# Performance work log

Hardware: AMD Instinct MI355X
Metric: run time of the kernel (lower is better)

Reference implementation:

```python
import jax, jax.numpy as jnp
import numpy as np

B, S, D = 4, 2048, 1024   # batch, seq_len, size
K = 4                     # max_choice
A = 2                     # activate_choice (== default forward choices)


def setup_inputs() -> dict:
    key = jax.random.key(0)
    ks = jax.random.split(key, 8)
    sc = 0.02  # weight init scale
    return {
        "x": jax.random.normal(ks[0], (B, S, D), jnp.float32),
        "Wm": jax.random.normal(ks[1], (A, D, D), jnp.float32) * sc,   # Memory expert weights
        "bm": jnp.zeros((A, D), jnp.float32),
        "ln_g": jnp.ones((D,), jnp.float32),                            # shared LayerNorm (self.lim)
        "ln_b": jnp.zeros((D,), jnp.float32),
        "Wg": jax.random.normal(ks[2], (D, K), jnp.float32) * sc,       # Linker gate
        "bg": jnp.zeros((K,), jnp.float32),
        "We": jax.random.normal(ks[3], (K, D, D), jnp.float32) * sc,    # Linker experts
        "be": jnp.zeros((K, D), jnp.float32),
        "Wfit": jax.random.normal(ks[4], ((A + 1) * D, D), jnp.float32) * sc,
        "bfit": jnp.zeros((D,), jnp.float32),
        "choices": A,
    }


def _layer_norm(x, g, b, eps=1e-5):
    m = jnp.mean(x, axis=-1, keepdims=True)
    v = jnp.mean((x - m) ** 2, axis=-1, keepdims=True)
    return (x - m) * jax.lax.rsqrt(v + eps) * g + b


def reference(x, Wm, bm, ln_g, ln_b, Wg, bg, We, be, Wfit, bfit, choices):
    # Triple-nested per-token loop vectorized: the in-place += means each
    # choice's Memory expert sees the x already updated by previous choices,
    # i.e. sequentially over `choices`: x <- x + LN(Memory_c(x)).
    for c in range(choices):
        mem = jnp.einsum('bsd,de->bse', x, Wm[c]) + bm[c]
        x = x + _layer_norm(mem, ln_g, ln_b)

    # Linker: gate over max_choice experts, pick top-`choices`, concat outputs.
    logits = jnp.einsum('bsd,dk->bsk', x, Wg) + bg          # [B,S,K]
    _, idx = jax.lax.top_k(logits, choices)                  # [B,S,A]
    eo = jnp.einsum('bsd,kde->bske', x, We) + be             # [B,S,K,D]
    sel = jnp.take_along_axis(eo, idx[..., None], axis=2)    # [B,S,A,D]
    link = sel.reshape(sel.shape[0], sel.shape[1], -1)       # [B,S,A*D]

    h = jnp.concatenate([link, x], axis=-1)                  # [B,S,(A+1)*D]
    h = jnp.einsum('bsf,fd->bsd', h, Wfit) + bfit
    h = _layer_norm(h, ln_g, ln_b)
    return jax.nn.gelu(h, approximate=False)
```

## Files before the change

kernel.cpp:

```cpp
#include <hip/hip_runtime.h>
#include <hip/hip_bf16.h>
#include <math.h>

typedef __bf16 bf16x8 __attribute__((ext_vector_type(8)));
typedef float  f32x4  __attribute__((ext_vector_type(4)));
typedef unsigned int   u32;
typedef unsigned short u16;
typedef u16 u16x8 __attribute__((ext_vector_type(8)));

#define D_ 1024
#define M_ 8192

static __device__ __forceinline__ u16 f2bf(float f) {
  u32 x = __float_as_uint(f);
  return (u16)((x + 0x7fffu + ((x >> 16) & 1u)) >> 16);
}
static __device__ __forceinline__ float bf2f(u16 s) {
  union { u32 b; float f; } u; u.b = ((u32)s) << 16; return u.f;
}
static __device__ __forceinline__ void gload16(const u16* g, u16* l) {
  __builtin_amdgcn_global_load_lds((const __attribute__((address_space(1))) u32*)g,
                                   (__attribute__((address_space(3))) u32*)l, 16, 0, 0);
}


__global__ __launch_bounds__(256) void pack_A_mem(const float* __restrict__ x, u16* __restrict__ dst) {
  int gid = blockIdx.x * 256 + threadIdx.x;
  int G = gid & 2047;
  int kblk = (gid >> 11) & 31;
  int mblk = gid >> 16;
  int rrow = G >> 3, gp = G & 7;
  int kg = gp ^ (rrow & 7);
  int region = kblk >> 4;
  int k = ((kblk & 15) * 8 + kg) * 8;
  const float* src = x + ((size_t)mblk * 256 + rrow) * D_ + k;
  f32x4 v0 = *reinterpret_cast<const f32x4*>(src);
  f32x4 v1 = *reinterpret_cast<const f32x4*>(src + 4);
  u16x8 o8;
#pragma unroll
  for (int j = 0; j < 4; ++j) {
    u16 h0 = f2bf(v0[j]); o8[j]     = region ? f2bf(v0[j] - bf2f(h0)) : h0;
    u16 h1 = f2bf(v1[j]); o8[4 + j] = region ? f2bf(v1[j] - bf2f(h1)) : h1;
  }
  *reinterpret_cast<u16x8*>(dst + (size_t)gid * 8) = o8;
}

__global__ __launch_bounds__(256) void pack_W_mem(const float* __restrict__ W, u16* __restrict__ dst) {
  __shared__ float tile[64][129];
  int bidx = blockIdx.x;
  int nt = bidx & 7, kt = (bidx >> 3) & 15, c = bidx >> 7;
  const float* Ws = W + ((size_t)c * D_ + kt * 64) * D_ + nt * 128;
#pragma unroll
  for (int rep = 0; rep < 32; ++rep) {
    int idx = rep * 256 + threadIdx.x;
    tile[idx >> 7][idx & 127] = Ws[(size_t)(idx >> 7) * D_ + (idx & 127)];
  }
  __syncthreads();
#pragma unroll
  for (int rep = 0; rep < 8; ++rep) {
    int gi = rep * 256 + threadIdx.x;
    int region = gi >> 10;
    int G = gi & 1023;
    int col = G >> 3, gp = G & 7;
    int kg = gp ^ (col & 7);
    u16x8 o8;
#pragma unroll
    for (int j = 0; j < 8; ++j) {
      float v = tile[kg * 8 + j][col];
      u16 h = f2bf(v);
      o8[j] = region ? f2bf(v - bf2f(h)) : h;
    }
    int kblk = region * 16 + kt;
    size_t off = ((((size_t)c * 8 + nt) * 32 + kblk) * 1024 + col * 8 + gp) * 8;
    *reinterpret_cast<u16x8*>(dst + off) = o8;
  }
}

__global__ __launch_bounds__(256) void pack_W_plain(const float* __restrict__ W, u16* __restrict__ dst, int KBLK) {
  __shared__ float tile[64][129];
  int bidx = blockIdx.x;
  int nt = bidx & 7;
  int t2 = bidx >> 3;
  int kt = t2 % KBLK;
  int e  = t2 / KBLK;
  const float* Ws = W + ((size_t)e * KBLK * 64 + kt * 64) * D_ + nt * 128;
#pragma unroll
  for (int rep = 0; rep < 32; ++rep) {
    int idx = rep * 256 + threadIdx.x;
    tile[idx >> 7][idx & 127] = Ws[(size_t)(idx >> 7) * D_ + (idx & 127)];
  }
  __syncthreads();
#pragma unroll
  for (int rep = 0; rep < 4; ++rep) {
    int gi = rep * 256 + threadIdx.x;
    int col = gi >> 3, gp = gi & 7;
    int kg = gp ^ (col & 7);
    u16x8 o8;
#pragma unroll
    for (int j = 0; j < 8; ++j) o8[j] = f2bf(tile[kg * 8 + j][col]);
    size_t off = ((((size_t)e * 8 + nt) * KBLK + kt) * 1024 + col * 8 + gp) * 8;
    *reinterpret_cast<u16x8*>(dst + off) = o8;
  }
}


__global__ __launch_bounds__(256) void ln1_pack(const float* __restrict__ xin, const float* __restrict__ mem,
                                                const float* __restrict__ bm, const float* __restrict__ g,
                                                const float* __restrict__ b, float* __restrict__ xout,
                                                u16* __restrict__ apack) {
  int row = blockIdx.x, tid = threadIdx.x;
  __shared__ float yrow[1024];
  __shared__ float red[8];
  f32x4 mv = *reinterpret_cast<const f32x4*>(mem + (size_t)row * D_ + tid * 4);
  f32x4 bi = *reinterpret_cast<const f32x4*>(bm + tid * 4);
  float a[4]; float s = 0.f, ss = 0.f;
#pragma unroll
  for (int i = 0; i < 4; ++i) { a[i] = mv[i] + bi[i]; s += a[i]; ss += a[i] * a[i]; }
#pragma unroll
  for (int o = 1; o < 64; o <<= 1) { s += __shfl_xor(s, o); ss += __shfl_xor(ss, o); }
  int wv = tid >> 6, ln = tid & 63;
  if (ln == 0) { red[wv] = s; red[4 + wv] = ss; }
  __syncthreads();
  float S = red[0] + red[1] + red[2] + red[3];
  float SS = red[4] + red[5] + red[6] + red[7];
  float mean = S * (1.f / 1024.f);
  float var = SS * (1.f / 1024.f) - mean * mean;
  float rs = rsqrtf(var + 1e-5f);
  f32x4 g4 = *reinterpret_cast<const f32x4*>(g + tid * 4);
  f32x4 b4 = *reinterpret_cast<const f32x4*>(b + tid * 4);
  f32x4 xv = *reinterpret_cast<const f32x4*>(xin + (size_t)row * D_ + tid * 4);
  f32x4 o4;
#pragma unroll
  for (int i = 0; i < 4; ++i) o4[i] = xv[i] + (a[i] - mean) * rs * g4[i] + b4[i];
  *reinterpret_cast<f32x4*>(xout + (size_t)row * D_ + tid * 4) = o4;
  *reinterpret_cast<f32x4*>(yrow + tid * 4) = o4;
  __syncthreads();
  int region = tid >> 7;
  int q = tid & 127;
  int kblk = region * 16 + (q >> 3);
  int kg = q & 7;
  int rrow = row & 255, mblk = row >> 8;
  const float* ys = yrow + q * 8;
  u16x8 o8;
#pragma unroll
  for (int j = 0; j < 8; ++j) {
    float v = ys[j]; u16 h = f2bf(v);
    o8[j] = region ? f2bf(v - bf2f(h)) : h;
  }
  size_t off = (((size_t)mblk * 32 + kblk) * 2048 + rrow * 8 + (kg ^ (rrow & 7))) * 8;
  *reinterpret_cast<u16x8*>(apack + off) = o8;
}

__global__ __launch_bounds__(256) void ln2_gate_pack(const float* __restrict__ xin, const float* __restrict__ mem,
                                                     const float* __restrict__ bm1, const float* __restrict__ g,
                                                     const float* __restrict__ b, const float* __restrict__ Wg,
                                                     const float* __restrict__ bg, u16* __restrict__ apack,
                                                     u16* __restrict__ hpack, int2* __restrict__ idx) {
  int row = blockIdx.x, tid = threadIdx.x;
  __shared__ float yrow[1024];
  __shared__ float red[8];
  __shared__ float gred[16];
  f32x4 mv = *reinterpret_cast<const f32x4*>(mem + (size_t)row * D_ + tid * 4);
  f32x4 bi = *reinterpret_cast<const f32x4*>(bm1 + tid * 4);
  float a[4]; float s = 0.f, ss = 0.f;
#pragma unroll
  for (int i = 0; i < 4; ++i) { a[i] = mv[i] + bi[i]; s += a[i]; ss += a[i] * a[i]; }
#pragma unroll
  for (int o = 1; o < 64; o <<= 1) { s += __shfl_xor(s, o); ss += __shfl_xor(ss, o); }
  int wv = tid >> 6, ln = tid & 63;
  if (ln == 0) { red[wv] = s; red[4 + wv] = ss; }
  __syncthreads();
  float S = red[0] + red[1] + red[2] + red[3];
  float SS = red[4] + red[5] + red[6] + red[7];
  float mean = S * (1.f / 1024.f);
  float var = SS * (1.f / 1024.f) - mean * mean;
  float rs = rsqrtf(var + 1e-5f);
  f32x4 g4 = *reinterpret_cast<const f32x4*>(g + tid * 4);
  f32x4 b4 = *reinterpret_cast<const f32x4*>(b + tid * 4);
  f32x4 xv = *reinterpret_cast<const f32x4*>(xin + (size_t)row * D_ + tid * 4);
  f32x4 o4;
#pragma unroll
  for (int i = 0; i < 4; ++i) o4[i] = xv[i] + (a[i] - mean) * rs * g4[i] + b4[i];
  *reinterpret_cast<f32x4*>(yrow + tid * 4) = o4;
  float p0 = 0.f, p1 = 0.f, p2 = 0.f, p3 = 0.f;
#pragma unroll
  for (int i = 0; i < 4; ++i) {
    f32x4 w = *reinterpret_cast<const f32x4*>(Wg + (size_t)(tid * 4 + i) * 4);
    p0 += o4[i] * w[0]; p1 += o4[i] * w[1]; p2 += o4[i] * w[2]; p3 += o4[i] * w[3];
  }
#pragma unroll
  for (int o = 1; o < 64; o <<= 1) {
    p0 += __shfl_xor(p0, o); p1 += __shfl_xor(p1, o);
    p2 += __shfl_xor(p2, o); p3 += __shfl_xor(p3, o);
  }
  if (ln == 0) { gred[wv * 4] = p0; gred[wv * 4 + 1] = p1; gred[wv * 4 + 2] = p2; gred[wv * 4 + 3] = p3; }
  __syncthreads();
  if (tid == 0) {
    float lg[4];
#pragma unroll
    for (int c = 0; c < 4; ++c) lg[c] = gred[c] + gred[4 + c] + gred[8 + c] + gred[12 + c] + bg[c];
    int i0 = 0; float v0 = lg[0];
#pragma unroll
    for (int k = 1; k < 4; ++k) if (lg[k] > v0) { v0 = lg[k]; i0 = k; }
    int i1 = -1; float v1 = -3.4e38f;
#pragma unroll
    for (int k = 0; k < 4; ++k) if (k != i0 && lg[k] > v1) { v1 = lg[k]; i1 = k; }
    idx[row] = make_int2(i0, i1);
  }
  int q = tid & 127;
  int kblk = q >> 3, kg = q & 7;
  int rrow = row & 255, mblk = row >> 8;
  const float* ys = yrow + q * 8;
  u16x8 o8;
#pragma unroll
  for (int j = 0; j < 8; ++j) o8[j] = f2bf(ys[j]);
  int pos = rrow * 8 + (kg ^ (rrow & 7));
  if (tid < 128) {
    *reinterpret_cast<u16x8*>(apack + (((size_t)mblk * 16 + kblk) * 2048 + pos) * 8) = o8;
  } else {
    *reinterpret_cast<u16x8*>(hpack + (((size_t)mblk * 48 + 32 + kblk) * 2048 + pos) * 8) = o8;
  }
}

__global__ __launch_bounds__(256) void final_ln_gelu(const float* __restrict__ fit, const float* __restrict__ bfit,
                                                     const float* __restrict__ g, const float* __restrict__ b,
                                                     float* __restrict__ out) {
  int row = blockIdx.x, tid = threadIdx.x;
  f32x4 hv = *reinterpret_cast<const f32x4*>(fit + (size_t)row * D_ + tid * 4);
  f32x4 bi = *reinterpret_cast<const f32x4*>(bfit + tid * 4);
  float a[4]; float s = 0.f, ss = 0.f;
#pragma unroll
  for (int i = 0; i < 4; ++i) { a[i] = hv[i] + bi[i]; s += a[i]; ss += a[i] * a[i]; }
#pragma unroll
  for (int o = 1; o < 64; o <<= 1) { s += __shfl_xor(s, o); ss += __shfl_xor(ss, o); }
  __shared__ float red[8];
  int wv = tid >> 6, ln = tid & 63;
  if (ln == 0) { red[wv] = s; red[4 + wv] = ss; }
  __syncthreads();
  float S = red[0] + red[1] + red[2] + red[3];
  float SS = red[4] + red[5] + red[6] + red[7];
  float mean = S * (1.f / 1024.f);
  float var = SS * (1.f / 1024.f) - mean * mean;
  float rs = rsqrtf(var + 1e-5f);
  f32x4 g4 = *reinterpret_cast<const f32x4*>(g + tid * 4);
  f32x4 b4 = *reinterpret_cast<const f32x4*>(b + tid * 4);
  f32x4 o4;
#pragma unroll
  for (int i = 0; i < 4; ++i) {
    float y = (a[i] - mean) * rs * g4[i] + b4[i];
    o4[i] = 0.5f * y * (1.f + erff(y * 0.70710678118654752f));
  }
  *reinterpret_cast<f32x4*>(out + (size_t)row * D_ + tid * 4) = o4;
}

#define MFMA(a, b, c) __builtin_amdgcn_mfma_f32_16x16x32_bf16(a, b, c, 0, 0, 0)

template<int MEMFOLD, int EPI>
__global__ __launch_bounds__(512, 1) void gemm8(const u16* __restrict__ A, const u16* __restrict__ B,
                                                float* __restrict__ C, u16* __restrict__ hp,
                                                const int2* __restrict__ idx, const float* __restrict__ be,
                                                int KIT, int AKB, int BKB) {
  __shared__ __align__(16) u16 lds[3][24576];
  const int tid = threadIdx.x;
  const int wid = tid >> 6, l = tid & 63;
  const int wm = wid >> 1, wn = wid & 1;
  const int lk = l >> 4, l15 = l & 15;
  const int bid = blockIdx.x;
  const int mblk = bid & 31;
  const int nblk = (bid >> 5) & 7;
  const int e    = bid >> 8;

  const u16* Ablob = A + (size_t)mblk * AKB * 16384;
  const u16* Bblob = B + ((size_t)e * 8 + nblk) * BKB * 8192;

  f32x4 acc[4][4];
#pragma unroll
  for (int i = 0; i < 4; ++i)
#pragma unroll
    for (int j = 0; j < 4; ++j) acc[i][j] = (f32x4){0.f, 0.f, 0.f, 0.f};

  auto amap = [&](int it) -> int {
    if (!MEMFOLD) return it;
    int kb = (int)((unsigned)it / 3u), sub = it - kb * 3;
    return kb + (sub == 2 ? 16 : 0);
  };
  auto bmap = [&](int it) -> int {
    if (!MEMFOLD) return it;
    int kb = (int)((unsigned)it / 3u), sub = it - kb * 3;
    return kb + (sub == 1 ? 16 : 0);
  };

  auto stageA0 = [&](int s, int it) {
    const u16* As = Ablob + (size_t)amap(it) * 16384;
#pragma unroll
    for (int r = 0; r < 3; ++r) {
      int u = r * 512 + tid;
      gload16(As + (size_t)u * 8, &lds[s][u * 8]);
    }
  };
  auto stageA1B = [&](int s, int it) {
    const u16* As = Ablob + (size_t)amap(it) * 16384;
    const u16* Bs = Bblob + (size_t)bmap(it) * 8192;
    int u = 3 * 512 + tid;
    gload16(As + (size_t)u * 8, &lds[s][u * 8]);
#pragma unroll
    for (int r = 0; r < 2; ++r) {
      int v = r * 512 + tid;
      gload16(Bs + (size_t)v * 8, &lds[s][16384 + v * 8]);
    }
  };
  auto ldA = [&](int s, int mi, int ks) -> bf16x8 {
    int r = wm * 64 + mi * 16 + l15;
    int gp = (ks * 4 + lk) ^ (r & 7);
    return *reinterpret_cast<const bf16x8*>(&lds[s][(r * 8 + gp) * 8]);
  };
  auto ldB = [&](int s, int ni, int ks) -> bf16x8 {
    int c = wn * 64 + ni * 16 + l15;
    int gp = (ks * 4 + lk) ^ (c & 7);
    return *reinterpret_cast<const bf16x8*>(&lds[s][16384 + (c * 8 + gp) * 8]);
  };

  stageA0(0, 0); stageA1B(0, 0);
  stageA0(1, 1); stageA1B(1, 1);
  asm volatile("s_waitcnt vmcnt(6)" ::: "memory");
  asm volatile("s_barrier" ::: "memory");

  int cur = 0;
  for (int t = 0; t < KIT; ++t) {
    int nxt = cur + 2; if (nxt >= 3) nxt -= 3;
    bool pf = (t + 2) < KIT;
    bf16x8 A0, A1, A2, A3, B0, B1, B2, B3;
    A0 = ldA(cur, 0, 0); A1 = ldA(cur, 1, 0); A2 = ldA(cur, 2, 0); A3 = ldA(cur, 3, 0);
    B0 = ldB(cur, 0, 0); B1 = ldB(cur, 1, 0); B2 = ldB(cur, 2, 0); B3 = ldB(cur, 3, 0);
    if (pf) stageA0(nxt, t + 2);
    __builtin_amdgcn_s_setprio(1);
    acc[0][0] = MFMA(A0, B0, acc[0][0]); acc[1][0] = MFMA(A1, B0, acc[1][0]);
    acc[2][0] = MFMA(A2, B0, acc[2][0]); acc[3][0] = MFMA(A3, B0, acc[3][0]);
    acc[0][1] = MFMA(A0, B1, acc[0][1]); acc[1][1] = MFMA(A1, B1, acc[1][1]);
    acc[2][1] = MFMA(A2, B1, acc[2][1]); acc[3][1] = MFMA(A3, B1, acc[3][1]);
    acc[0][2] = MFMA(A0, B2, acc[0][2]); acc[1][2] = MFMA(A1, B2, acc[1][2]);
    acc[2][2] = MFMA(A2, B2, acc[2][2]); acc[3][2] = MFMA(A3, B2, acc[3][2]);
    acc[0][3] = MFMA(A0, B3, acc[0][3]); acc[1][3] = MFMA(A1, B3, acc[1][3]);
    acc[2][3] = MFMA(A2, B3, acc[2][3]); acc[3][3] = MFMA(A3, B3, acc[3][3]);
    __builtin_amdgcn_s_setprio(0);
    asm volatile("s_barrier" ::: "memory");
    A0 = ldA(cur, 0, 1); A1 = ldA(cur, 1, 1); A2 = ldA(cur, 2, 1); A3 = ldA(cur, 3, 1);
    B0 = ldB(cur, 0, 1); B1 = ldB(cur, 1, 1); B2 = ldB(cur, 2, 1); B3 = ldB(cur, 3, 1);
    if (pf) stageA1B(nxt, t + 2);
    __builtin_amdgcn_s_setprio(1);
    acc[0][0] = MFMA(A0, B0, acc[0][0]); acc[1][0] = MFMA(A1, B0, acc[1][0]);
    acc[2][0] = MFMA(A2, B0, acc[2][0]); acc[3][0] = MFMA(A3, B0, acc[3][0]);
    acc[0][1] = MFMA(A0, B1, acc[0][1]); acc[1][1] = MFMA(A1, B1, acc[1][1]);
    acc[2][1] = MFMA(A2, B1, acc[2][1]); acc[3][1] = MFMA(A3, B1, acc[3][1]);
    acc[0][2] = MFMA(A0, B2, acc[0][2]); acc[1][2] = MFMA(A1, B2, acc[1][2]);
    acc[2][2] = MFMA(A2, B2, acc[2][2]); acc[3][2] = MFMA(A3, B2, acc[3][2]);
    acc[0][3] = MFMA(A0, B3, acc[0][3]); acc[1][3] = MFMA(A1, B3, acc[1][3]);
    acc[2][3] = MFMA(A2, B3, acc[2][3]); acc[3][3] = MFMA(A3, B3, acc[3][3]);
    __builtin_amdgcn_s_setprio(0);
    if (pf) { asm volatile("s_waitcnt vmcnt(6)" ::: "memory"); }
    else    { asm volatile("s_waitcnt vmcnt(0)" ::: "memory"); }
    asm volatile("s_barrier" ::: "memory");
    cur += 1; if (cur >= 3) cur -= 3;
  }

  if (EPI == 0) {
#pragma unroll
    for (int mi = 0; mi < 4; ++mi) {
#pragma unroll
      for (int jj = 0; jj < 4; ++jj) {
        int row = mblk * 256 + wm * 64 + mi * 16 + lk * 4 + jj;
        float* Crow = C + (size_t)row * D_ + nblk * 128 + wn * 64 + l15;
#pragma unroll
        for (int ni = 0; ni < 4; ++ni) Crow[ni * 16] = acc[mi][ni][jj];
      }
    }
  } else {
#pragma unroll
    for (int mi = 0; mi < 4; ++mi) {
      int rbase = mblk * 256 + wm * 64 + mi * 16 + lk * 4;
      int2 rid[4];
#pragma unroll
      for (int jj = 0; jj < 4; ++jj) rid[jj] = idx[rbase + jj];
#pragma unroll
      for (int ni = 0; ni < 4; ++ni) {
        int col = nblk * 128 + wn * 64 + ni * 16 + l15;
        float bev = be[(size_t)e * D_ + col];
#pragma unroll
        for (int jj = 0; jj < 4; ++jj) {
          int slot = (rid[jj].x == e) ? 0 : ((rid[jj].y == e) ? 1 : -1);
          if (slot >= 0) {
            int row = rbase + jj;
            int rrow = row & 255;
            int kh = slot * D_ + col;
            int kblk = kh >> 6;
            int kg = (kh >> 3) & 7;
            size_t off = (((size_t)mblk * 48 + kblk) * 2048 + rrow * 8 + (kg ^ (rrow & 7))) * 8 + (kh & 7);
            hp[off] = f2bf(acc[mi][ni][jj] + bev);
          }
        }
      }
    }
  }
}

extern "C" void kernel_launch(void* const* d_in, const int* in_sizes, int n_in,
                              void* d_out, int out_size, void* d_ws, size_t ws_size,
                              hipStream_t stream) {
  const float* x_in = (const float*)d_in[0];
  const float* Wm   = (const float*)d_in[1];
  const float* bm   = (const float*)d_in[2];
  const float* ln_g = (const float*)d_in[3];
  const float* ln_b = (const float*)d_in[4];
  const float* Wg   = (const float*)d_in[5];
  const float* bg   = (const float*)d_in[6];
  const float* We   = (const float*)d_in[7];
  const float* be   = (const float*)d_in[8];
  const float* Wfit = (const float*)d_in[9];
  const float* bfit = (const float*)d_in[10];
  float* out = (float*)d_out;

  char* ws = (char*)d_ws;
  size_t off = 0;
  auto alloc = [&](size_t bytes) -> void* {
    void* p = ws + off; off += (bytes + 255) & ~(size_t)255; return p;
  };
  float* x1      = (float*)alloc((size_t)M_ * D_ * 4);
  float* memb    = (float*)alloc((size_t)M_ * D_ * 4);
  u16* AmemPack  = (u16*)alloc((size_t)32 * 32 * 2048 * 16);
  u16* AplainPk  = (u16*)alloc((size_t)32 * 16 * 2048 * 16);
  u16* Hpack     = (u16*)alloc((size_t)32 * 48 * 2048 * 16);
  u16* WmPack    = (u16*)alloc((size_t)2 * 8 * 32 * 1024 * 16);
  u16* WePack    = (u16*)alloc((size_t)4 * 8 * 16 * 1024 * 16);
  u16* WfPack    = (u16*)alloc((size_t)8 * 48 * 1024 * 16);
  int2* idxb     = (int2*)alloc((size_t)M_ * 8);

  pack_W_mem  <<<256, 256, 0, stream>>>(Wm, WmPack);
  pack_W_plain<<<512, 256, 0, stream>>>(We, WePack, 16);
  pack_W_plain<<<384, 256, 0, stream>>>(Wfit, WfPack, 48);

  pack_A_mem<<<8192, 256, 0, stream>>>(x_in, AmemPack);
  gemm8<1, 0><<<256, 512, 0, stream>>>(AmemPack, WmPack, memb, nullptr, nullptr, nullptr, 48, 32, 32);
  ln1_pack<<<8192, 256, 0, stream>>>(x_in, memb, bm, ln_g, ln_b, x1, AmemPack);
  gemm8<1, 0><<<256, 512, 0, stream>>>(AmemPack, WmPack + (size_t)2097152, memb,
                                       nullptr, nullptr, nullptr, 48, 32, 32);
  ln2_gate_pack<<<8192, 256, 0, stream>>>(x1, memb, bm + D_, ln_g, ln_b, Wg, bg, AplainPk, Hpack, idxb);

  gemm8<0, 1><<<1024, 512, 0, stream>>>(AplainPk, WePack, nullptr, Hpack, idxb, be, 16, 16, 16);

  gemm8<0, 0><<<256, 512, 0, stream>>>(Hpack, WfPack, memb, nullptr, nullptr, nullptr, 48, 48, 48);

  final_ln_gelu<<<8192, 256, 0, stream>>>(memb, bfit, ln_g, ln_b, out);
}
```

Before: 424.6 us.

## Split GEMM tile staging into four chunks interleaved with MFMA phases

Replaces the two prefetch stages per K-iteration with four smaller chunks (two A halves and two B pieces). Each chunk is issued between finer-grained MFMA groups, and B fragment LDS reads are split so that only two B fragments are loaded before each half of the MFMAs. The goal is to spread global-to-LDS traffic and LDS reads more evenly across the compute, so the matrix units are fed more steadily. In exchange, each iteration now has several extra s_barrier and lgkmcnt(0) waits, which could add synchronisation stalls.

```diff
diff --git a/kernel.cpp b/kernel.cpp
--- a/kernel.cpp
+++ b/kernel.cpp
@@ -290,22 +290,16 @@
     return kb + (sub == 1 ? 16 : 0);
   };
 
-  auto stageA0 = [&](int s, int it) {
-    const u16* As = Ablob + (size_t)amap(it) * 16384;
-#pragma unroll
-    for (int r = 0; r < 3; ++r) {
-      int u = r * 512 + tid;
-      gload16(As + (size_t)u * 8, &lds[s][u * 8]);
-    }
-  };
-  auto stageA1B = [&](int s, int it) {
-    const u16* As = Ablob + (size_t)amap(it) * 16384;
-    const u16* Bs = Bblob + (size_t)bmap(it) * 8192;
-    int u = 3 * 512 + tid;
-    gload16(As + (size_t)u * 8, &lds[s][u * 8]);
-#pragma unroll
-    for (int r = 0; r < 2; ++r) {
-      int v = r * 512 + tid;
+  auto stageChunk = [&](int s, int it, int c) {
+    if (c <= 1) {
+      const u16* As = Ablob + (size_t)amap(it) * 16384;
+      int u0 = c * 1024 + tid;
+      int u1 = u0 + 512;
+      gload16(As + (size_t)u0 * 8, &lds[s][u0 * 8]);
+      gload16(As + (size_t)u1 * 8, &lds[s][u1 * 8]);
+    } else {
+      const u16* Bs = Bblob + (size_t)bmap(it) * 8192;
+      int v = (c - 2) * 512 + tid;
       gload16(Bs + (size_t)v * 8, &lds[s][16384 + v * 8]);
     }
   };
@@ -320,8 +314,8 @@
     return *reinterpret_cast<const bf16x8*>(&lds[s][16384 + (c * 8 + gp) * 8]);
   };
 
-  stageA0(0, 0); stageA1B(0, 0);
-  stageA0(1, 1); stageA1B(1, 1);
+  stageChunk(0, 0, 0); stageChunk(0, 0, 1); stageChunk(0, 0, 2); stageChunk(0, 0, 3);
+  stageChunk(1, 1, 0); stageChunk(1, 1, 1); stageChunk(1, 1, 2); stageChunk(1, 1, 3);
   asm volatile("s_waitcnt vmcnt(6)" ::: "memory");
   asm volatile("s_barrier" ::: "memory");
 
@@ -331,13 +325,22 @@
     bool pf = (t + 2) < KIT;
     bf16x8 A0, A1, A2, A3, B0, B1, B2, B3;
     A0 = ldA(cur, 0, 0); A1 = ldA(cur, 1, 0); A2 = ldA(cur, 2, 0); A3 = ldA(cur, 3, 0);
-    B0 = ldB(cur, 0, 0); B1 = ldB(cur, 1, 0); B2 = ldB(cur, 2, 0); B3 = ldB(cur, 3, 0);
-    if (pf) stageA0(nxt, t + 2);
+    B0 = ldB(cur, 0, 0); B1 = ldB(cur, 1, 0);
+    if (pf) stageChunk(nxt, t + 2, 0);
+    asm volatile("s_barrier" ::: "memory");
+    asm volatile("s_waitcnt lgkmcnt(0)" ::: "memory");
     __builtin_amdgcn_s_setprio(1);
     acc[0][0] = MFMA(A0, B0, acc[0][0]); acc[1][0] = MFMA(A1, B0, acc[1][0]);
     acc[2][0] = MFMA(A2, B0, acc[2][0]); acc[3][0] = MFMA(A3, B0, acc[3][0]);
     acc[0][1] = MFMA(A0, B1, acc[0][1]); acc[1][1] = MFMA(A1, B1, acc[1][1]);
     acc[2][1] = MFMA(A2, B1, acc[2][1]); acc[3][1] = MFMA(A3, B1, acc[3][1]);
+    __builtin_amdgcn_s_setprio(0);
+    asm volatile("s_barrier" ::: "memory");
+    B2 = ldB(cur, 2, 0); B3 = ldB(cur, 3, 0);
+    if (pf) stageChunk(nxt, t + 2, 1);
+    asm volatile("s_barrier" ::: "memory");
+    asm volatile("s_waitcnt lgkmcnt(0)" ::: "memory");
+    __builtin_amdgcn_s_setprio(1);
     acc[0][2] = MFMA(A0, B2, acc[0][2]); acc[1][2] = MFMA(A1, B2, acc[1][2]);
     acc[2][2] = MFMA(A2, B2, acc[2][2]); acc[3][2] = MFMA(A3, B2, acc[3][2]);
     acc[0][3] = MFMA(A0, B3, acc[0][3]); acc[1][3] = MFMA(A1, B3, acc[1][3]);
@@ -345,13 +348,22 @@
     __builtin_amdgcn_s_setprio(0);
     asm volatile("s_barrier" ::: "memory");
     A0 = ldA(cur, 0, 1); A1 = ldA(cur, 1, 1); A2 = ldA(cur, 2, 1); A3 = ldA(cur, 3, 1);
-    B0 = ldB(cur, 0, 1); B1 = ldB(cur, 1, 1); B2 = ldB(cur, 2, 1); B3 = ldB(cur, 3, 1);
-    if (pf) stageA1B(nxt, t + 2);
+    B0 = ldB(cur, 0, 1); B1 = ldB(cur, 1, 1);
+    if (pf) stageChunk(nxt, t + 2, 2);
+    asm volatile("s_barrier" ::: "memory");
+    asm volatile("s_waitcnt lgkmcnt(0)" ::: "memory");
     __builtin_amdgcn_s_setprio(1);
     acc[0][0] = MFMA(A0, B0, acc[0][0]); acc[1][0] = MFMA(A1, B0, acc[1][0]);
     acc[2][0] = MFMA(A2, B0, acc[2][0]); acc[3][0] = MFMA(A3, B0, acc[3][0]);
     acc[0][1] = MFMA(A0, B1, acc[0][1]); acc[1][1] = MFMA(A1, B1, acc[1][1]);
     acc[2][1] = MFMA(A2, B1, acc[2][1]); acc[3][1] = MFMA(A3, B1, acc[3][1]);
+    __builtin_amdgcn_s_setprio(0);
+    asm volatile("s_barrier" ::: "memory");
+    B2 = ldB(cur, 2, 1); B3 = ldB(cur, 3, 1);
+    if (pf) stageChunk(nxt, t + 2, 3);
+    asm volatile("s_barrier" ::: "memory");
+    asm volatile("s_waitcnt lgkmcnt(0)" ::: "memory");
+    __builtin_amdgcn_s_setprio(1);
     acc[0][2] = MFMA(A0, B2, acc[0][2]); acc[1][2] = MFMA(A1, B2, acc[1][2]);
     acc[2][2] = MFMA(A2, B2, acc[2][2]); acc[3][2] = MFMA(A3, B2, acc[3][2]);
     acc[0][3] = MFMA(A0, B3, acc[0][3]); acc[1][3] = MFMA(A1, B3, acc[1][3]);
```

Result: slower. 452.4 us (+6.6%).

## Replace 256x128 triple-buffered GEMM with 128x128 single-buffer 4-wave tiles

Applied to the files above, without the earlier changes.

Shrinks the GEMM tile from 256x128 with 8 waves and a three-stage LDS pipeline to 128x128 with 4 waves, one LDS buffer and two blocks per CU. The block count doubles (512, or 2048 for the expert GEMM), and A is addressed as half of the existing 256-row packed blob. The goal is better occupancy and wave balance across the 256 CUs, relying on two co-resident blocks to hide latency instead of explicit prefetching. It drops the software pipelining, since every K step now waits on its global loads behind __syncthreads, and each weight tile is loaded twice as often.

```diff
diff --git a/kernel.cpp b/kernel.cpp
--- a/kernel.cpp
+++ b/kernel.cpp
@@ -256,21 +256,22 @@
 #define MFMA(a, b, c) __builtin_amdgcn_mfma_f32_16x16x32_bf16(a, b, c, 0, 0, 0)
 
 template<int MEMFOLD, int EPI>
-__global__ __launch_bounds__(512, 1) void gemm8(const u16* __restrict__ A, const u16* __restrict__ B,
+__global__ __launch_bounds__(256, 2) void gemm4(const u16* __restrict__ A, const u16* __restrict__ B,
                                                 float* __restrict__ C, u16* __restrict__ hp,
                                                 const int2* __restrict__ idx, const float* __restrict__ be,
                                                 int KIT, int AKB, int BKB) {
-  __shared__ __align__(16) u16 lds[3][24576];
+  __shared__ __align__(16) u16 lds[16384];
   const int tid = threadIdx.x;
   const int wid = tid >> 6, l = tid & 63;
   const int wm = wid >> 1, wn = wid & 1;
   const int lk = l >> 4, l15 = l & 15;
   const int bid = blockIdx.x;
-  const int mblk = bid & 31;
-  const int nblk = (bid >> 5) & 7;
-  const int e    = bid >> 8;
-
-  const u16* Ablob = A + (size_t)mblk * AKB * 16384;
+  const int mblk = bid & 63;
+  const int nblk = (bid >> 6) & 7;
+  const int e    = bid >> 9;
+  const int half = mblk & 1;
+
+  const u16* Ablob = A + (size_t)(mblk >> 1) * AKB * 16384 + (size_t)half * 8192;
   const u16* Bblob = B + ((size_t)e * 8 + nblk) * BKB * 8192;
 
   f32x4 acc[4][4];
@@ -290,77 +291,43 @@
     return kb + (sub == 1 ? 16 : 0);
   };
 
-  auto stageA0 = [&](int s, int it) {
-    const u16* As = Ablob + (size_t)amap(it) * 16384;
-#pragma unroll
-    for (int r = 0; r < 3; ++r) {
-      int u = r * 512 + tid;
-      gload16(As + (size_t)u * 8, &lds[s][u * 8]);
-    }
-  };
-  auto stageA1B = [&](int s, int it) {
-    const u16* As = Ablob + (size_t)amap(it) * 16384;
-    const u16* Bs = Bblob + (size_t)bmap(it) * 8192;
-    int u = 3 * 512 + tid;
-    gload16(As + (size_t)u * 8, &lds[s][u * 8]);
-#pragma unroll
-    for (int r = 0; r < 2; ++r) {
-      int v = r * 512 + tid;
-      gload16(Bs + (size_t)v * 8, &lds[s][16384 + v * 8]);
-    }
-  };
-  auto ldA = [&](int s, int mi, int ks) -> bf16x8 {
+  auto ldA = [&](int mi, int ks) -> bf16x8 {
     int r = wm * 64 + mi * 16 + l15;
     int gp = (ks * 4 + lk) ^ (r & 7);
-    return *reinterpret_cast<const bf16x8*>(&lds[s][(r * 8 + gp) * 8]);
+    return *reinterpret_cast<const bf16x8*>(&lds[(r * 8 + gp) * 8]);
   };
-  auto ldB = [&](int s, int ni, int ks) -> bf16x8 {
+  auto ldB = [&](int ni, int ks) -> bf16x8 {
     int c = wn * 64 + ni * 16 + l15;
     int gp = (ks * 4 + lk) ^ (c & 7);
-    return *reinterpret_cast<const bf16x8*>(&lds[s][16384 + (c * 8 + gp) * 8]);
+    return *reinterpret_cast<const bf16x8*>(&lds[8192 + (c * 8 + gp) * 8]);
   };
 
-  stageA0(0, 0); stageA1B(0, 0);
-  stageA0(1, 1); stageA1B(1, 1);
-  asm volatile("s_waitcnt vmcnt(6)" ::: "memory");
-  asm volatile("s_barrier" ::: "memory");
-
-  int cur = 0;
   for (int t = 0; t < KIT; ++t) {
-    int nxt = cur + 2; if (nxt >= 3) nxt -= 3;
-    bool pf = (t + 2) < KIT;
-    bf16x8 A0, A1, A2, A3, B0, B1, B2, B3;
-    A0 = ldA(cur, 0, 0); A1 = ldA(cur, 1, 0); A2 = ldA(cur, 2, 0); A3 = ldA(cur, 3, 0);
-    B0 = ldB(cur, 0, 0); B1 = ldB(cur, 1, 0); B2 = ldB(cur, 2, 0); B3 = ldB(cur, 3, 0);
-    if (pf) stageA0(nxt, t + 2);
-    __builtin_amdgcn_s_setprio(1);
-    acc[0][0] = MFMA(A0, B0, acc[0][0]); acc[1][0] = MFMA(A1, B0, acc[1][0]);
-    acc[2][0] = MFMA(A2, B0, acc[2][0]); acc[3][0] = MFMA(A3, B0, acc[3][0]);
-    acc[0][1] = MFMA(A0, B1, acc[0][1]); acc[1][1] = MFMA(A1, B1, acc[1][1]);
-    acc[2][1] = MFMA(A2, B1, acc[2][1]); acc[3][1] = MFMA(A3, B1, acc[3][1]);
-    acc[0][2] = MFMA(A0, B2, acc[0][2]); acc[1][2] = MFMA(A1, B2, acc[1][2]);
-    acc[2][2] = MFMA(A2, B2, acc[2][2]); acc[3][2] = MFMA(A3, B2, acc[3][2]);
-    acc[0][3] = MFMA(A0, B3, acc[0][3]); acc[1][3] = MFMA(A1, B3, acc[1][3]);
-    acc[2][3] = MFMA(A2, B3, acc[2][3]); acc[3][3] = MFMA(A3, B3, acc[3][3]);
-    __builtin_amdgcn_s_setprio(0);
-    asm volatile("s_barrier" ::: "memory");
-    A0 = ldA(cur, 0, 1); A1 = ldA(cur, 1, 1); A2 = ldA(cur, 2, 1); A3 = ldA(cur, 3, 1);
-    B0 = ldB(cur, 0, 1); B1 = ldB(cur, 1, 1); B2 = ldB(cur, 2, 1); B3 = ldB(cur, 3, 1);
-    if (pf) stageA1B(nxt, t + 2);
-    __builtin_amdgcn_s_setprio(1);
-    acc[0][0] = MFMA(A0, B0, acc[0][0]); acc[1][0] = MFMA(A1, B0, acc[1][0]);
-    acc[2][0] = MFMA(A2, B0, acc[2][0]); acc[3][0] = MFMA(A3, B0, acc[3][0]);
-    acc[0][1] = MFMA(A0, B1, acc[0][1]); acc[1][1] = MFMA(A1, B1, acc[1][1]);
-    acc[2][1] = MFMA(A2, B1, acc[2][1]); acc[3][1] = MFMA(A3, B1, acc[3][1]);
-    acc[0][2] = MFMA(A0, B2, acc[0][2]); acc[1][2] = MFMA(A1, B2, acc[1][2]);
-    acc[2][2] = MFMA(A2, B2, acc[2][2]); acc[3][2] = MFMA(A3, B2, acc[3][2]);
-    acc[0][3] = MFMA(A0, B3, acc[0][3]); acc[1][3] = MFMA(A1, B3, acc[1][3]);
-    acc[2][3] = MFMA(A2, B3, acc[2][3]); acc[3][3] = MFMA(A3, B3, acc[3][3]);
-    __builtin_amdgcn_s_setprio(0);
-    if (pf) { asm volatile("s_waitcnt vmcnt(6)" ::: "memory"); }
-    else    { asm volatile("s_waitcnt vmcnt(0)" ::: "memory"); }
-    asm volatile("s_barrier" ::: "memory");
-    cur += 1; if (cur >= 3) cur -= 3;
+    const u16* As = Ablob + (size_t)amap(t) * 16384;
+    const u16* Bs = Bblob + (size_t)bmap(t) * 8192;
+#pragma unroll
+    for (int i = 0; i < 4; ++i) {
+      int u = i * 256 + tid;
+      gload16(As + (size_t)u * 8, &lds[u * 8]);
+      gload16(Bs + (size_t)u * 8, &lds[8192 + u * 8]);
+    }
+    __syncthreads();
+#pragma unroll
+    for (int ks = 0; ks < 2; ++ks) {
+      bf16x8 A0 = ldA(0, ks), A1 = ldA(1, ks), A2 = ldA(2, ks), A3 = ldA(3, ks);
+      bf16x8 B0 = ldB(0, ks), B1 = ldB(1, ks), B2 = ldB(2, ks), B3 = ldB(3, ks);
+      __builtin_amdgcn_s_setprio(1);
+      acc[0][0] = MFMA(A0, B0, acc[0][0]); acc[1][0] = MFMA(A1, B0, acc[1][0]);
+      acc[2][0] = MFMA(A2, B0, acc[2][0]); acc[3][0] = MFMA(A3, B0, acc[3][0]);
+      acc[0][1] = MFMA(A0, B1, acc[0][1]); acc[1][1] = MFMA(A1, B1, acc[1][1]);
+      acc[2][1] = MFMA(A2, B1, acc[2][1]); acc[3][1] = MFMA(A3, B1, acc[3][1]);
+      acc[0][2] = MFMA(A0, B2, acc[0][2]); acc[1][2] = MFMA(A1, B2, acc[1][2]);
+      acc[2][2] = MFMA(A2, B2, acc[2][2]); acc[3][2] = MFMA(A3, B2, acc[3][2]);
+      acc[0][3] = MFMA(A0, B3, acc[0][3]); acc[1][3] = MFMA(A1, B3, acc[1][3]);
+      acc[2][3] = MFMA(A2, B3, acc[2][3]); acc[3][3] = MFMA(A3, B3, acc[3][3]);
+      __builtin_amdgcn_s_setprio(0);
+    }
+    __syncthreads();
   }
 
   if (EPI == 0) {
@@ -368,7 +335,7 @@
     for (int mi = 0; mi < 4; ++mi) {
 #pragma unroll
       for (int jj = 0; jj < 4; ++jj) {
-        int row = mblk * 256 + wm * 64 + mi * 16 + lk * 4 + jj;
+        int row = mblk * 128 + wm * 64 + mi * 16 + lk * 4 + jj;
         float* Crow = C + (size_t)row * D_ + nblk * 128 + wn * 64 + l15;
 #pragma unroll
         for (int ni = 0; ni < 4; ++ni) Crow[ni * 16] = acc[mi][ni][jj];
@@ -377,7 +344,7 @@
   } else {
 #pragma unroll
     for (int mi = 0; mi < 4; ++mi) {
-      int rbase = mblk * 256 + wm * 64 + mi * 16 + lk * 4;
+      int rbase = mblk * 128 + wm * 64 + mi * 16 + lk * 4;
       int2 rid[4];
 #pragma unroll
       for (int jj = 0; jj < 4; ++jj) rid[jj] = idx[rbase + jj];
@@ -390,11 +357,12 @@
           int slot = (rid[jj].x == e) ? 0 : ((rid[jj].y == e) ? 1 : -1);
           if (slot >= 0) {
             int row = rbase + jj;
+            int hmblk = row >> 8;
             int rrow = row & 255;
             int kh = slot * D_ + col;
             int kblk = kh >> 6;
             int kg = (kh >> 3) & 7;
-            size_t off = (((size_t)mblk * 48 + kblk) * 2048 + rrow * 8 + (kg ^ (rrow & 7))) * 8 + (kh & 7);
+            size_t off = (((size_t)hmblk * 48 + kblk) * 2048 + rrow * 8 + (kg ^ (rrow & 7))) * 8 + (kh & 7);
             hp[off] = f2bf(acc[mi][ni][jj] + bev);
           }
         }
@@ -439,15 +407,15 @@
   pack_W_plain<<<384, 256, 0, stream>>>(Wfit, WfPack, 48);
 
   pack_A_mem<<<8192, 256, 0, stream>>>(x_in, AmemPack);
-  gemm8<1, 0><<<256, 512, 0, stream>>>(AmemPack, WmPack, memb, nullptr, nullptr, nullptr, 48, 32, 32);
+  gemm4<1, 0><<<512, 256, 0, stream>>>(AmemPack, WmPack, memb, nullptr, nullptr, nullptr, 48, 32, 32);
   ln1_pack<<<8192, 256, 0, stream>>>(x_in, memb, bm, ln_g, ln_b, x1, AmemPack);
-  gemm8<1, 0><<<256, 512, 0, stream>>>(AmemPack, WmPack + (size_t)2097152, memb,
+  gemm4<1, 0><<<512, 256, 0, stream>>>(AmemPack, WmPack + (size_t)2097152, memb,
                                        nullptr, nullptr, nullptr, 48, 32, 32);
   ln2_gate_pack<<<8192, 256, 0, stream>>>(x1, memb, bm + D_, ln_g, ln_b, Wg, bg, AplainPk, Hpack, idxb);
 
-  gemm8<0, 1><<<1024, 512, 0, stream>>>(AplainPk, WePack, nullptr, Hpack, idxb, be, 16, 16, 16);
-
-  gemm8<0, 0><<<256, 512, 0, stream>>>(Hpack, WfPack, memb, nullptr, nullptr, nullptr, 48, 48, 48);
+  gemm4<0, 1><<<2048, 256, 0, stream>>>(AplainPk, WePack, nullptr, Hpack, idxb, be, 16, 16, 16);
+
+  gemm4<0, 0><<<512, 256, 0, stream>>>(Hpack, WfPack, memb, nullptr, nullptr, nullptr, 48, 48, 48);
 
   final_ln_gelu<<<8192, 256, 0, stream>>>(memb, bfit, ln_g, ln_b, out);
 }
```

New measurement: 436.4 us. 1.03x slower.
